# Performance work log

Measured on AMD Instinct MI355X. Metric: run time of the kernel, lower is better.

Reference implementation:

```python
import jax, jax.numpy as jnp
import numpy as np

N, H, S = 2048, 512, 256

def setup_inputs() -> dict:
    key = jax.random.key(0)
    k1, k2, k3 = jax.random.split(key, 3)
    hidden_states = jax.random.normal(k1, (N, H, S), dtype=jnp.float32)
    # xavier_uniform-ish scale for W and context vector
    limW = float(np.sqrt(6.0 / (H + H)))
    attention_weights = jax.random.uniform(k2, (H, H), dtype=jnp.float32, minval=-limW, maxval=limW)
    attention_bias = jnp.zeros((H, 1), dtype=jnp.float32)
    limc = float(np.sqrt(6.0 / (H + 1)))
    context_vector = jax.random.uniform(k3, (H, 1), dtype=jnp.float32, minval=-limc, maxval=limc)
    return {
        "hidden_states": hidden_states,
        "attention_weights": attention_weights,
        "attention_bias": attention_bias,
        "context_vector": context_vector,
    }

def reference(hidden_states, attention_weights, attention_bias, context_vector):
    # hidden_states: (N, H, S)
    hs_t = jnp.swapaxes(hidden_states, 1, 2)              # (N, S, H)
    score = jnp.tanh(hs_t @ attention_weights + attention_bias[:, 0])  # (N, S, H)
    alignment = (score @ context_vector)[..., 0]          # (N, S)
    attn = jax.nn.softmax(alignment, axis=1)              # (N, S)
    context = jnp.einsum('ns,nhs->nh', attn, hidden_states)  # (N, H)
    return context
```

## Files before the change

kernel.cpp:

```cpp
#include <hip/hip_runtime.h>
#include <hip/hip_bf16.h>
#include <stdint.h>
#include <stddef.h>

typedef __attribute__((ext_vector_type(8))) short short8;
typedef __attribute__((ext_vector_type(4))) float f32x4;

#define NB 2048
#define HD 512
#define SD 256

__device__ __forceinline__ short f2bf(float x) {
  __hip_bfloat16 h = __float2bfloat16(x);
  return *reinterpret_cast<short*>(&h);
}

__device__ __forceinline__ float fast_tanh(float x) {
  x = fminf(fmaxf(x, -15.f), 15.f);
  float e = __expf(2.f * x);
  return __fdividef(e - 1.f, e + 1.f);
}

__global__ __launch_bounds__(256) void wconv_kernel(const float* __restrict__ W,
                                                    short* __restrict__ Wtb) {
  __shared__ float tile[32][33];
  const int bx = blockIdx.x;
  const int tk0 = (bx & 15) * 32;
  const int tj0 = (bx >> 4) * 32;
  const int lx = threadIdx.x & 31;
  const int ly = threadIdx.x >> 5;
  for (int r = 0; r < 4; ++r) {
    int yy = ly + r * 8;
    tile[yy][lx] = W[(size_t)(tk0 + yy) * HD + tj0 + lx];
  }
  __syncthreads();
  const int kb = tk0 >> 5;
  for (int r = 0; r < 4; ++r) {
    int yy = ly + r * 8;
    Wtb[(size_t)kb * (HD * 32) + (size_t)(tj0 + yy) * 32 + lx] = f2bf(tile[lx][yy]);
  }
}

__global__ void __launch_bounds__(256, 2)
align_kernel(const float* __restrict__ hs, const short* __restrict__ Wtb,
             const float* __restrict__ bias, const float* __restrict__ ctx,
             float* __restrict__ align_out)
{
  __shared__ float abuf[64];

  const int tid = threadIdx.x;
  const int n = blockIdx.x >> 2;
  const int s0 = (blockIdx.x & 3) * 64;
  const int lane = tid & 63;
  const int wid = tid >> 6;
  const int l15 = lane & 15;
  const int lg = lane >> 4;
  const int jb = wid * 128;

  if (tid < 64) abuf[tid] = 0.f;
  __syncthreads();

  const float* hsA = hs + (size_t)n * (HD * SD) + s0 + l15 + (size_t)(lg * 8) * SD;
  const short* wbase = Wtb + (size_t)(jb + l15) * 32 + lg * 8;

  f32x4 acc[4][8];
  #pragma unroll
  for (int i = 0; i < 4; ++i)
    #pragma unroll
    for (int p = 0; p < 8; ++p)
      acc[i][p] = (f32x4){0.f, 0.f, 0.f, 0.f};

  for (int kt = 0; kt < 16; ++kt) {
    short8 wf[8];
    const short* wk = wbase + (size_t)kt * (HD * 32);
    #pragma unroll
    for (int p = 0; p < 8; ++p)
      wf[p] = *(const short8*)(wk + p * (16 * 32));

    short8 af[4];
    const float* ak = hsA + (size_t)(kt * 32) * SD;
    #pragma unroll
    for (int i = 0; i < 4; ++i) {
      float v[8];
      #pragma unroll
      for (int e = 0; e < 8; ++e)
        v[e] = ak[(size_t)e * SD + i * 16];
      short8 pk;
      #pragma unroll
      for (int e = 0; e < 8; ++e) pk[e] = f2bf(v[e]);
      af[i] = pk;
    }

    #pragma unroll
    for (int i = 0; i < 4; ++i)
      #pragma unroll
      for (int p = 0; p < 8; ++p)
        acc[i][p] = __builtin_amdgcn_mfma_f32_16x16x32_bf16(wf[p], af[i], acc[i][p], 0, 0, 0);
  }

  float part[4] = {0.f, 0.f, 0.f, 0.f};
  #pragma unroll
  for (int p = 0; p < 8; ++p) {
    const int j = jb + p * 16 + lg * 4;
    f32x4 bv = *(const f32x4*)(bias + j);
    f32x4 cv = *(const f32x4*)(ctx + j);
    #pragma unroll
    for (int i = 0; i < 4; ++i)
      #pragma unroll
      for (int r = 0; r < 4; ++r)
        part[i] += fast_tanh(acc[i][p][r] + bv[r]) * cv[r];
  }
  #pragma unroll
  for (int i = 0; i < 4; ++i) {
    part[i] += __shfl_xor(part[i], 16);
    part[i] += __shfl_xor(part[i], 32);
  }
  if (lg == 0) {
    #pragma unroll
    for (int i = 0; i < 4; ++i)
      atomicAdd(&abuf[i * 16 + l15], part[i]);
  }
  __syncthreads();
  if (tid < 64) align_out[(size_t)n * SD + s0 + tid] = abuf[tid];
}

__global__ __launch_bounds__(256) void ctx_kernel(const float* __restrict__ hs,
                                                  const float* __restrict__ align_in,
                                                  float* __restrict__ out)
{
  __shared__ __align__(16) float attn_s[256];
  __shared__ float red[8];
  const int n = blockIdx.x;
  const int t = threadIdx.x;
  const int lane = t & 63, wid = t >> 6;

  float a = align_in[(size_t)n * 256 + t];
  float m = a;
  #pragma unroll
  for (int off = 32; off; off >>= 1) m = fmaxf(m, __shfl_xor(m, off));
  if (lane == 0) red[wid] = m;
  __syncthreads();
  m = fmaxf(fmaxf(red[0], red[1]), fmaxf(red[2], red[3]));
  float e = __expf(a - m);
  float s = e;
  #pragma unroll
  for (int off = 32; off; off >>= 1) s += __shfl_xor(s, off);
  if (lane == 0) red[4 + wid] = s;
  __syncthreads();
  s = red[4] + red[5] + red[6] + red[7];
  attn_s[t] = e / s;
  __syncthreads();

  const int grp = t & 7;
  const int hrow = t >> 3;
  float av[32];
  #pragma unroll
  for (int u = 0; u < 8; ++u) {
    float4 v = *(const float4*)&attn_s[grp * 32 + u * 4];
    av[4*u+0] = v.x; av[4*u+1] = v.y; av[4*u+2] = v.z; av[4*u+3] = v.w;
  }
  const float* hb = hs + (size_t)n * (HD * SD) + grp * 32;
  for (int it = 0; it < 16; ++it) {
    const int h = it * 32 + hrow;
    const float4* p = (const float4*)(hb + (size_t)h * SD);
    float acc = 0.f;
    #pragma unroll
    for (int u = 0; u < 8; ++u) {
      float4 v = p[u];
      acc += av[4*u+0]*v.x + av[4*u+1]*v.y + av[4*u+2]*v.z + av[4*u+3]*v.w;
    }
    acc += __shfl_xor(acc, 1);
    acc += __shfl_xor(acc, 2);
    acc += __shfl_xor(acc, 4);
    if (grp == 0) out[(size_t)n * HD + h] = acc;
  }
}

extern "C" void kernel_launch(void* const* d_in, const int* in_sizes, int n_in,
                              void* d_out, int out_size, void* d_ws, size_t ws_size,
                              hipStream_t stream) {
  (void)in_sizes; (void)n_in; (void)out_size; (void)ws_size;
  const float* hs = (const float*)d_in[0];
  const float* W  = (const float*)d_in[1];
  const float* b  = (const float*)d_in[2];
  const float* c  = (const float*)d_in[3];
  float* out = (float*)d_out;

  float* align_ws = (float*)d_ws;
  short* Wtb = (short*)((char*)d_ws + (size_t)NB * SD * 4);

  wconv_kernel<<<256, 256, 0, stream>>>(W, Wtb);
  align_kernel<<<NB * 4, 256, 0, stream>>>(hs, Wtb, b, c, align_ws);
  ctx_kernel<<<NB, 256, 0, stream>>>(hs, align_ws, out);
}
```

Before: 846.8 us.

## Pre-transpose hidden states to bf16 (N,S,H) and double-buffer the align MFMA loop

Adds a tiled transpose kernel that converts hidden_states to a bf16 (N,S,H) workspace buffer. The alignment kernel can then load contiguous short8 fragments instead of doing strided scalar fp32 loads and per-element conversion. The MFMA k-loop is also double-buffered so the next tile's fragments load while the current tile computes. The cost is an extra full pass over the input (a 1 GB read plus a 0.5 GB write) and a large workspace requirement. When the workspace is too small, the code falls back to a chunked path or to the original kernel.

```diff
diff --git a/kernel.cpp b/kernel.cpp
--- a/kernel.cpp
+++ b/kernel.cpp
@@ -41,13 +41,142 @@
   }
 }
 
+__global__ __launch_bounds__(256) void tconv_kernel(const float* __restrict__ hs,
+                                                    short* __restrict__ hst,
+                                                    int nbase) {
+  __shared__ float tile[64][65];
+  const int bx = blockIdx.x;
+  const int nl = bx >> 5;
+  const int n = nbase + nl;
+  const int h0 = ((bx >> 2) & 7) * 64;
+  const int s0 = (bx & 3) * 64;
+  const int t = threadIdx.x;
+
+  const int lh = t >> 2;
+  const int lq = t & 3;
+  const float* src = hs + (size_t)n * (HD * SD) + (size_t)(h0 + lh) * SD + s0;
+  #pragma unroll
+  for (int r = 0; r < 4; ++r) {
+    const int q = lq + r * 4;
+    float4 v = *(const float4*)(src + q * 4);
+    tile[lh][q * 4 + 0] = v.x;
+    tile[lh][q * 4 + 1] = v.y;
+    tile[lh][q * 4 + 2] = v.z;
+    tile[lh][q * 4 + 3] = v.w;
+  }
+  __syncthreads();
+
+  const int ls = t >> 2;
+  const int lo = t & 3;
+  short* dst = hst + (size_t)nl * (SD * HD) + (size_t)(s0 + ls) * HD + h0;
+  #pragma unroll
+  for (int r = 0; r < 2; ++r) {
+    const int oct = lo + r * 4;
+    short8 pk;
+    #pragma unroll
+    for (int e = 0; e < 8; ++e)
+      pk[e] = f2bf(tile[oct * 8 + e][ls]);
+    *(short8*)(dst + oct * 8) = pk;
+  }
+}
+
 __global__ void __launch_bounds__(256, 2)
-align_kernel(const float* __restrict__ hs, const short* __restrict__ Wtb,
-             const float* __restrict__ bias, const float* __restrict__ ctx,
-             float* __restrict__ align_out)
+align_fast(const short* __restrict__ hst, const short* __restrict__ Wtb,
+           const float* __restrict__ bias, const float* __restrict__ ctx,
+           float* __restrict__ align_out, int nbase)
 {
   __shared__ float abuf[64];
 
+  const int tid = threadIdx.x;
+  const int nl = blockIdx.x >> 2;
+  const int n = nbase + nl;
+  const int s0 = (blockIdx.x & 3) * 64;
+  const int lane = tid & 63;
+  const int wid = tid >> 6;
+  const int l15 = lane & 15;
+  const int lg = lane >> 4;
+  const int jb = wid * 128;
+
+  if (tid < 64) abuf[tid] = 0.f;
+  __syncthreads();
+
+  const short* aBase = hst + (size_t)nl * (SD * HD) + (size_t)(s0 + l15) * HD + lg * 8;
+  const short* wBase = Wtb + (size_t)(jb + l15) * 32 + lg * 8;
+
+  f32x4 acc[4][8];
+  #pragma unroll
+  for (int i = 0; i < 4; ++i)
+    #pragma unroll
+    for (int p = 0; p < 8; ++p)
+      acc[i][p] = (f32x4){0.f, 0.f, 0.f, 0.f};
+
+  short8 afA[4], wfA[8], afB[4], wfB[8];
+  #pragma unroll
+  for (int i = 0; i < 4; ++i) afA[i] = *(const short8*)(aBase + i * 16 * HD);
+  #pragma unroll
+  for (int p = 0; p < 8; ++p) wfA[p] = *(const short8*)(wBase + p * (16 * 32));
+
+  for (int kt = 0; kt < 16; kt += 2) {
+    {
+      const short* ak = aBase + (kt + 1) * 32;
+      #pragma unroll
+      for (int i = 0; i < 4; ++i) afB[i] = *(const short8*)(ak + i * 16 * HD);
+      const short* wk = wBase + (size_t)(kt + 1) * (HD * 32);
+      #pragma unroll
+      for (int p = 0; p < 8; ++p) wfB[p] = *(const short8*)(wk + p * (16 * 32));
+    }
+    #pragma unroll
+    for (int i = 0; i < 4; ++i)
+      #pragma unroll
+      for (int p = 0; p < 8; ++p)
+        acc[i][p] = __builtin_amdgcn_mfma_f32_16x16x32_bf16(wfA[p], afA[i], acc[i][p], 0, 0, 0);
+    if (kt < 14) {
+      const short* ak = aBase + (kt + 2) * 32;
+      #pragma unroll
+      for (int i = 0; i < 4; ++i) afA[i] = *(const short8*)(ak + i * 16 * HD);
+      const short* wk = wBase + (size_t)(kt + 2) * (HD * 32);
+      #pragma unroll
+      for (int p = 0; p < 8; ++p) wfA[p] = *(const short8*)(wk + p * (16 * 32));
+    }
+    #pragma unroll
+    for (int i = 0; i < 4; ++i)
+      #pragma unroll
+      for (int p = 0; p < 8; ++p)
+        acc[i][p] = __builtin_amdgcn_mfma_f32_16x16x32_bf16(wfB[p], afB[i], acc[i][p], 0, 0, 0);
+  }
+
+  float part[4] = {0.f, 0.f, 0.f, 0.f};
+  #pragma unroll
+  for (int p = 0; p < 8; ++p) {
+    const int j = jb + p * 16 + lg * 4;
+    f32x4 bv = *(const f32x4*)(bias + j);
+    f32x4 cv = *(const f32x4*)(ctx + j);
+    #pragma unroll
+    for (int i = 0; i < 4; ++i)
+      #pragma unroll
+      for (int r = 0; r < 4; ++r)
+        part[i] += fast_tanh(acc[i][p][r] + bv[r]) * cv[r];
+  }
+  #pragma unroll
+  for (int i = 0; i < 4; ++i) {
+    part[i] += __shfl_xor(part[i], 16);
+    part[i] += __shfl_xor(part[i], 32);
+  }
+  if (lg == 0) {
+    #pragma unroll
+    for (int i = 0; i < 4; ++i)
+      atomicAdd(&abuf[i * 16 + l15], part[i]);
+  }
+  __syncthreads();
+  if (tid < 64) align_out[(size_t)n * SD + s0 + tid] = abuf[tid];
+}
+
+__global__ void __launch_bounds__(256, 2)
+align_fallback(const float* __restrict__ hs, const short* __restrict__ Wtb,
+               const float* __restrict__ bias, const float* __restrict__ ctx,
+               float* __restrict__ align_out)
+{
+  __shared__ float abuf[64];
   const int tid = threadIdx.x;
   const int n = blockIdx.x >> 2;
   const int s0 = (blockIdx.x & 3) * 64;
@@ -179,17 +308,37 @@
 extern "C" void kernel_launch(void* const* d_in, const int* in_sizes, int n_in,
                               void* d_out, int out_size, void* d_ws, size_t ws_size,
                               hipStream_t stream) {
-  (void)in_sizes; (void)n_in; (void)out_size; (void)ws_size;
+  (void)in_sizes; (void)n_in; (void)out_size;
   const float* hs = (const float*)d_in[0];
   const float* W  = (const float*)d_in[1];
   const float* b  = (const float*)d_in[2];
   const float* c  = (const float*)d_in[3];
   float* out = (float*)d_out;
 
-  float* align_ws = (float*)d_ws;
-  short* Wtb = (short*)((char*)d_ws + (size_t)NB * SD * 4);
+  const size_t OFF_ALIGN = 0;
+  const size_t OFF_WTB   = (size_t)NB * SD * 4;
+  const size_t OFF_HST   = OFF_WTB + (size_t)16 * HD * 32 * 2;
+  const size_t HST_FULL  = (size_t)NB * SD * HD * 2;
+  const size_t HST_CHUNK = HST_FULL / 8;
+
+  float* align_ws = (float*)((char*)d_ws + OFF_ALIGN);
+  short* Wtb = (short*)((char*)d_ws + OFF_WTB);
+  short* hst = (short*)((char*)d_ws + OFF_HST);
 
   wconv_kernel<<<256, 256, 0, stream>>>(W, Wtb);
-  align_kernel<<<NB * 4, 256, 0, stream>>>(hs, Wtb, b, c, align_ws);
+
+  if (ws_size >= OFF_HST + HST_FULL) {
+    tconv_kernel<<<NB * 32, 256, 0, stream>>>(hs, hst, 0);
+    align_fast<<<NB * 4, 256, 0, stream>>>(hst, Wtb, b, c, align_ws, 0);
+  } else if (ws_size >= OFF_HST + HST_CHUNK) {
+    for (int chunk = 0; chunk < 8; ++chunk) {
+      const int nbase = chunk * (NB / 8);
+      tconv_kernel<<<(NB / 8) * 32, 256, 0, stream>>>(hs, hst, nbase);
+      align_fast<<<(NB / 8) * 4, 256, 0, stream>>>(hst, Wtb, b, c, align_ws, nbase);
+    }
+  } else {
+    align_fallback<<<NB * 4, 256, 0, stream>>>(hs, Wtb, b, c, align_ws);
+  }
+
   ctx_kernel<<<NB, 256, 0, stream>>>(hs, align_ws, out);
 }
```

Result: slower. 1.265 ms (+49.4%).

## Stage hidden-state and weight tiles in LDS with double buffering in align kernel

Applied to the files above, without the earlier changes.

The align kernel now uses 1024-thread blocks covering 128 sequence positions and all 512 output columns. Each k-step's bf16 activation tile and weight tile are loaded cooperatively into double-buffered shared memory, so every global element is fetched once per block instead of once per wave. The next tile's global loads are issued before the current tile's MFMAs. This cuts redundant global traffic for W and gives coalesced staging of hs, at the cost of a block-wide barrier every k-step and about 80KB of LDS per block, which may limit occupancy.

```diff
diff --git a/kernel.cpp b/kernel.cpp
--- a/kernel.cpp
+++ b/kernel.cpp
@@ -4,6 +4,7 @@
 #include <stddef.h>
 
 typedef __attribute__((ext_vector_type(8))) short short8;
+typedef __attribute__((ext_vector_type(4))) short short4v;
 typedef __attribute__((ext_vector_type(4))) float f32x4;
 
 #define NB 2048
@@ -41,69 +42,104 @@
   }
 }
 
-__global__ void __launch_bounds__(256, 2)
+__global__ void __launch_bounds__(1024, 4)
 align_kernel(const float* __restrict__ hs, const short* __restrict__ Wtb,
-             const float* __restrict__ bias, const float* __restrict__ ctx,
+             const float* __restrict__ bias, const float* __restrict__ ctxv,
              float* __restrict__ align_out)
 {
-  __shared__ float abuf[64];
+  __shared__ short As[2][128 * 32];
+  __shared__ short Ws[2][512 * 32];
+  __shared__ float abuf[128];
 
   const int tid = threadIdx.x;
-  const int n = blockIdx.x >> 2;
-  const int s0 = (blockIdx.x & 3) * 64;
+  const int n = blockIdx.x >> 1;
+  const int s0 = (blockIdx.x & 1) * 128;
+  const float* hsn = hs + (size_t)n * (HD * SD) + s0;
+
+  if (tid < 128) abuf[tid] = 0.f;
+
+  const int a_s = tid >> 3;
+  const int a_o = (tid >> 1) & 3;
+  const int a_h = tid & 1;
+  const int a_k = a_o * 8 + a_h * 4;
+  const int w_j = tid >> 1;
+  const int w_o = (tid & 1) * 2;
+
+  {
+    const float* src = hsn + (size_t)a_k * SD + a_s;
+    short4v pk;
+    #pragma unroll
+    for (int e = 0; e < 4; ++e) pk[e] = f2bf(src[(size_t)e * SD]);
+    *(short4v*)&As[0][a_s * 32 + a_k] = pk;
+
+    const short* wsrc = Wtb + (size_t)w_j * 32 + w_o * 8;
+    *(short8*)&Ws[0][w_j * 32 + w_o * 8] = *(const short8*)(wsrc);
+    *(short8*)&Ws[0][w_j * 32 + w_o * 8 + 8] = *(const short8*)(wsrc + 8);
+  }
+  __syncthreads();
+
   const int lane = tid & 63;
   const int wid = tid >> 6;
+  const int wm = wid >> 3;
+  const int wj = wid & 7;
   const int l15 = lane & 15;
   const int lg = lane >> 4;
-  const int jb = wid * 128;
-
-  if (tid < 64) abuf[tid] = 0.f;
-  __syncthreads();
-
-  const float* hsA = hs + (size_t)n * (HD * SD) + s0 + l15 + (size_t)(lg * 8) * SD;
-  const short* wbase = Wtb + (size_t)(jb + l15) * 32 + lg * 8;
-
-  f32x4 acc[4][8];
+
+  f32x4 acc[4][4];
   #pragma unroll
   for (int i = 0; i < 4; ++i)
     #pragma unroll
-    for (int p = 0; p < 8; ++p)
+    for (int p = 0; p < 4; ++p)
       acc[i][p] = (f32x4){0.f, 0.f, 0.f, 0.f};
 
+  const int aoff = (wm * 64 + l15) * 32 + lg * 8;
+  const int woff = (wj * 64 + l15) * 32 + lg * 8;
+
   for (int kt = 0; kt < 16; ++kt) {
-    short8 wf[8];
-    const short* wk = wbase + (size_t)kt * (HD * 32);
-    #pragma unroll
-    for (int p = 0; p < 8; ++p)
-      wf[p] = *(const short8*)(wk + p * (16 * 32));
-
-    short8 af[4];
-    const float* ak = hsA + (size_t)(kt * 32) * SD;
+    const int cur = kt & 1;
+
+    float av[4];
+    short8 wv0, wv1;
+    if (kt < 15) {
+      const float* src = hsn + (size_t)((kt + 1) * 32 + a_k) * SD + a_s;
+      #pragma unroll
+      for (int e = 0; e < 4; ++e) av[e] = src[(size_t)e * SD];
+      const short* wsrc = Wtb + (size_t)(kt + 1) * (HD * 32) + w_j * 32 + w_o * 8;
+      wv0 = *(const short8*)(wsrc);
+      wv1 = *(const short8*)(wsrc + 8);
+    }
+
+    short8 wf[4];
+    #pragma unroll
+    for (int p = 0; p < 4; ++p)
+      wf[p] = *(const short8*)&Ws[cur][woff + p * (16 * 32)];
+
     #pragma unroll
     for (int i = 0; i < 4; ++i) {
-      float v[8];
-      #pragma unroll
-      for (int e = 0; e < 8; ++e)
-        v[e] = ak[(size_t)e * SD + i * 16];
-      short8 pk;
-      #pragma unroll
-      for (int e = 0; e < 8; ++e) pk[e] = f2bf(v[e]);
-      af[i] = pk;
-    }
-
-    #pragma unroll
-    for (int i = 0; i < 4; ++i)
-      #pragma unroll
-      for (int p = 0; p < 8; ++p)
-        acc[i][p] = __builtin_amdgcn_mfma_f32_16x16x32_bf16(wf[p], af[i], acc[i][p], 0, 0, 0);
+      short8 af = *(const short8*)&As[cur][aoff + i * (16 * 32)];
+      #pragma unroll
+      for (int p = 0; p < 4; ++p)
+        acc[i][p] = __builtin_amdgcn_mfma_f32_16x16x32_bf16(wf[p], af, acc[i][p], 0, 0, 0);
+    }
+
+    if (kt < 15) {
+      const int nxt = cur ^ 1;
+      short4v pk;
+      #pragma unroll
+      for (int e = 0; e < 4; ++e) pk[e] = f2bf(av[e]);
+      *(short4v*)&As[nxt][a_s * 32 + a_k] = pk;
+      *(short8*)&Ws[nxt][w_j * 32 + w_o * 8] = wv0;
+      *(short8*)&Ws[nxt][w_j * 32 + w_o * 8 + 8] = wv1;
+    }
+    __syncthreads();
   }
 
   float part[4] = {0.f, 0.f, 0.f, 0.f};
   #pragma unroll
-  for (int p = 0; p < 8; ++p) {
-    const int j = jb + p * 16 + lg * 4;
+  for (int p = 0; p < 4; ++p) {
+    const int j = wj * 64 + p * 16 + lg * 4;
     f32x4 bv = *(const f32x4*)(bias + j);
-    f32x4 cv = *(const f32x4*)(ctx + j);
+    f32x4 cv = *(const f32x4*)(ctxv + j);
     #pragma unroll
     for (int i = 0; i < 4; ++i)
       #pragma unroll
@@ -118,10 +154,10 @@
   if (lg == 0) {
     #pragma unroll
     for (int i = 0; i < 4; ++i)
-      atomicAdd(&abuf[i * 16 + l15], part[i]);
-  }
-  __syncthreads();
-  if (tid < 64) align_out[(size_t)n * SD + s0 + tid] = abuf[tid];
+      atomicAdd(&abuf[wm * 64 + i * 16 + l15], part[i]);
+  }
+  __syncthreads();
+  if (tid < 128) align_out[(size_t)n * SD + s0 + tid] = abuf[tid];
 }
 
 __global__ __launch_bounds__(256) void ctx_kernel(const float* __restrict__ hs,
@@ -190,6 +226,6 @@
   short* Wtb = (short*)((char*)d_ws + (size_t)NB * SD * 4);
 
   wconv_kernel<<<256, 256, 0, stream>>>(W, Wtb);
-  align_kernel<<<NB * 4, 256, 0, stream>>>(hs, Wtb, b, c, align_ws);
+  align_kernel<<<NB * 2, 1024, 0, stream>>>(hs, Wtb, b, c, align_ws);
   ctx_kernel<<<NB, 256, 0, stream>>>(hs, align_ws, out);
 }
```

Result: slower. 944.7 us (median of 2 runs) (+11.6%).

## Stage A and W tiles in double-buffered LDS and use 32x32x16 MFMA

Applied to the files above, without the earlier changes.

The align kernel now runs 512 threads per block and stages bf16-converted hidden-state and weight K-slices in double-buffered shared memory. The next slice is prefetched into registers while the current one feeds 32x32x16 MFMAs, and the weight layout is re-blocked into K groups of 16. This replaces per-wave direct global loads, with their redundant W fetches and strided hs reads, by cooperative loads and LDS reuse. In exchange it adds a barrier every K step, doubles the K iterations, and uses more LDS, which may limit occupancy.

```diff
diff --git a/kernel.cpp b/kernel.cpp
--- a/kernel.cpp
+++ b/kernel.cpp
@@ -4,11 +4,16 @@
 #include <stddef.h>
 
 typedef __attribute__((ext_vector_type(8))) short short8;
+typedef __attribute__((ext_vector_type(4))) short short4v;
 typedef __attribute__((ext_vector_type(4))) float f32x4;
+typedef __attribute__((ext_vector_type(16))) float f32x16;
 
 #define NB 2048
 #define HD 512
 #define SD 256
+
+#define AS_STR 24
+#define WS_STR 24
 
 __device__ __forceinline__ short f2bf(float x) {
   __hip_bfloat16 h = __float2bfloat16(x);
@@ -22,7 +27,7 @@
 }
 
 __global__ __launch_bounds__(256) void wconv_kernel(const float* __restrict__ W,
-                                                    short* __restrict__ Wtb) {
+                                                    short* __restrict__ Wtb16) {
   __shared__ float tile[32][33];
   const int bx = blockIdx.x;
   const int tk0 = (bx & 15) * 32;
@@ -34,91 +39,129 @@
     tile[yy][lx] = W[(size_t)(tk0 + yy) * HD + tj0 + lx];
   }
   __syncthreads();
-  const int kb = tk0 >> 5;
   for (int r = 0; r < 4; ++r) {
     int yy = ly + r * 8;
-    Wtb[(size_t)kb * (HD * 32) + (size_t)(tj0 + yy) * 32 + lx] = f2bf(tile[lx][yy]);
-  }
-}
-
-__global__ void __launch_bounds__(256, 2)
-align_kernel(const float* __restrict__ hs, const short* __restrict__ Wtb,
-             const float* __restrict__ bias, const float* __restrict__ ctx,
+    const int k = tk0 + lx;
+    Wtb16[(size_t)(k >> 4) * (HD * 16) + (size_t)(tj0 + yy) * 16 + (k & 15)] =
+        f2bf(tile[lx][yy]);
+  }
+}
+
+__global__ void __launch_bounds__(512, 4)
+align_kernel(const float* __restrict__ hs, const short* __restrict__ Wtb16,
+             const float* __restrict__ bias, const float* __restrict__ ctxv,
              float* __restrict__ align_out)
 {
+  __shared__ short As[2][64 * AS_STR];
+  __shared__ short Ws[2][512 * WS_STR];
   __shared__ float abuf[64];
 
   const int tid = threadIdx.x;
   const int n = blockIdx.x >> 2;
   const int s0 = (blockIdx.x & 3) * 64;
+  const float* hsn = hs + (size_t)n * (HD * SD) + s0;
+
+  if (tid < 64) abuf[tid] = 0.f;
+
+  const int a_s = tid & 63;
+  const int a_kq = (tid >> 6) & 3;
+  const int w_j = tid;
+
+  if (tid < 256) {
+    const float* src = hsn + (size_t)(a_kq * 4) * SD + a_s;
+    short4v pk;
+    pk[0] = f2bf(src[0]); pk[1] = f2bf(src[SD]);
+    pk[2] = f2bf(src[2 * SD]); pk[3] = f2bf(src[3 * SD]);
+    *(short4v*)&As[0][a_s * AS_STR + a_kq * 4] = pk;
+  }
+  {
+    const short* wsrc = Wtb16 + (size_t)w_j * 16;
+    *(short8*)&Ws[0][w_j * WS_STR] = *(const short8*)wsrc;
+    *(short8*)&Ws[0][w_j * WS_STR + 8] = *(const short8*)(wsrc + 8);
+  }
+  __syncthreads();
+
   const int lane = tid & 63;
   const int wid = tid >> 6;
-  const int l15 = lane & 15;
-  const int lg = lane >> 4;
-  const int jb = wid * 128;
-
-  if (tid < 64) abuf[tid] = 0.f;
-  __syncthreads();
-
-  const float* hsA = hs + (size_t)n * (HD * SD) + s0 + l15 + (size_t)(lg * 8) * SD;
-  const short* wbase = Wtb + (size_t)(jb + l15) * 32 + lg * 8;
-
-  f32x4 acc[4][8];
-  #pragma unroll
-  for (int i = 0; i < 4; ++i)
+  const int jb = wid * 64;
+  const int l31 = lane & 31;
+  const int hg = lane >> 5;
+
+  f32x16 acc[2][2];
+  #pragma unroll
+  for (int i = 0; i < 2; ++i)
     #pragma unroll
-    for (int p = 0; p < 8; ++p)
-      acc[i][p] = (f32x4){0.f, 0.f, 0.f, 0.f};
-
-  for (int kt = 0; kt < 16; ++kt) {
-    short8 wf[8];
-    const short* wk = wbase + (size_t)kt * (HD * 32);
+    for (int p = 0; p < 2; ++p)
+      #pragma unroll
+      for (int q = 0; q < 16; ++q) acc[i][p][q] = 0.f;
+
+  const int afo = l31 * AS_STR + hg * 8;
+  const int wfo = (jb + l31) * WS_STR + hg * 8;
+
+  for (int kt = 0; kt < 32; ++kt) {
+    const int cur = kt & 1;
+
+    float av[4];
+    short8 wv0, wv1;
+    if (kt < 31) {
+      if (tid < 256) {
+        const float* src = hsn + (size_t)((kt + 1) * 16 + a_kq * 4) * SD + a_s;
+        #pragma unroll
+        for (int e = 0; e < 4; ++e) av[e] = src[(size_t)e * SD];
+      }
+      const short* wsrc = Wtb16 + (size_t)(kt + 1) * (HD * 16) + (size_t)w_j * 16;
+      wv0 = *(const short8*)wsrc;
+      wv1 = *(const short8*)(wsrc + 8);
+    }
+
+    short8 wf0 = *(const short8*)&Ws[cur][wfo];
+    short8 wf1 = *(const short8*)&Ws[cur][wfo + 32 * WS_STR];
+    short8 af0 = *(const short8*)&As[cur][afo];
+    short8 af1 = *(const short8*)&As[cur][afo + 32 * AS_STR];
+
+    __builtin_amdgcn_s_setprio(1);
+    acc[0][0] = __builtin_amdgcn_mfma_f32_32x32x16_bf16(wf0, af0, acc[0][0], 0, 0, 0);
+    acc[0][1] = __builtin_amdgcn_mfma_f32_32x32x16_bf16(wf1, af0, acc[0][1], 0, 0, 0);
+    acc[1][0] = __builtin_amdgcn_mfma_f32_32x32x16_bf16(wf0, af1, acc[1][0], 0, 0, 0);
+    acc[1][1] = __builtin_amdgcn_mfma_f32_32x32x16_bf16(wf1, af1, acc[1][1], 0, 0, 0);
+    __builtin_amdgcn_s_setprio(0);
+
+    if (kt < 31) {
+      const int nxt = cur ^ 1;
+      if (tid < 256) {
+        short4v pk;
+        #pragma unroll
+        for (int e = 0; e < 4; ++e) pk[e] = f2bf(av[e]);
+        *(short4v*)&As[nxt][a_s * AS_STR + a_kq * 4] = pk;
+      }
+      *(short8*)&Ws[nxt][w_j * WS_STR] = wv0;
+      *(short8*)&Ws[nxt][w_j * WS_STR + 8] = wv1;
+    }
+    __syncthreads();
+  }
+
+  float part0 = 0.f, part1 = 0.f;
+  #pragma unroll
+  for (int p = 0; p < 2; ++p) {
+    const int jfr = jb + p * 32 + hg * 4;
     #pragma unroll
-    for (int p = 0; p < 8; ++p)
-      wf[p] = *(const short8*)(wk + p * (16 * 32));
-
-    short8 af[4];
-    const float* ak = hsA + (size_t)(kt * 32) * SD;
-    #pragma unroll
-    for (int i = 0; i < 4; ++i) {
-      float v[8];
+    for (int g = 0; g < 4; ++g) {
+      const int j4 = jfr + g * 8;
+      f32x4 bv = *(const f32x4*)(bias + j4);
+      f32x4 cv = *(const f32x4*)(ctxv + j4);
       #pragma unroll
-      for (int e = 0; e < 8; ++e)
-        v[e] = ak[(size_t)e * SD + i * 16];
-      short8 pk;
-      #pragma unroll
-      for (int e = 0; e < 8; ++e) pk[e] = f2bf(v[e]);
-      af[i] = pk;
-    }
-
-    #pragma unroll
-    for (int i = 0; i < 4; ++i)
-      #pragma unroll
-      for (int p = 0; p < 8; ++p)
-        acc[i][p] = __builtin_amdgcn_mfma_f32_16x16x32_bf16(wf[p], af[i], acc[i][p], 0, 0, 0);
-  }
-
-  float part[4] = {0.f, 0.f, 0.f, 0.f};
-  #pragma unroll
-  for (int p = 0; p < 8; ++p) {
-    const int j = jb + p * 16 + lg * 4;
-    f32x4 bv = *(const f32x4*)(bias + j);
-    f32x4 cv = *(const f32x4*)(ctx + j);
-    #pragma unroll
-    for (int i = 0; i < 4; ++i)
-      #pragma unroll
-      for (int r = 0; r < 4; ++r)
-        part[i] += fast_tanh(acc[i][p][r] + bv[r]) * cv[r];
-  }
-  #pragma unroll
-  for (int i = 0; i < 4; ++i) {
-    part[i] += __shfl_xor(part[i], 16);
-    part[i] += __shfl_xor(part[i], 32);
-  }
-  if (lg == 0) {
-    #pragma unroll
-    for (int i = 0; i < 4; ++i)
-      atomicAdd(&abuf[i * 16 + l15], part[i]);
+      for (int r = 0; r < 4; ++r) {
+        const int q = g * 4 + r;
+        part0 += fast_tanh(acc[0][p][q] + bv[r]) * cv[r];
+        part1 += fast_tanh(acc[1][p][q] + bv[r]) * cv[r];
+      }
+    }
+  }
+  part0 += __shfl_xor(part0, 32);
+  part1 += __shfl_xor(part1, 32);
+  if (lane < 32) {
+    atomicAdd(&abuf[l31], part0);
+    atomicAdd(&abuf[32 + l31], part1);
   }
   __syncthreads();
   if (tid < 64) align_out[(size_t)n * SD + s0 + tid] = abuf[tid];
@@ -187,9 +230,9 @@
   float* out = (float*)d_out;
 
   float* align_ws = (float*)d_ws;
-  short* Wtb = (short*)((char*)d_ws + (size_t)NB * SD * 4);
-
-  wconv_kernel<<<256, 256, 0, stream>>>(W, Wtb);
-  align_kernel<<<NB * 4, 256, 0, stream>>>(hs, Wtb, b, c, align_ws);
+  short* Wtb16 = (short*)((char*)d_ws + (size_t)NB * SD * 4);
+
+  wconv_kernel<<<256, 256, 0, stream>>>(W, Wtb16);
+  align_kernel<<<NB * 4, 512, 0, stream>>>(hs, Wtb16, b, c, align_ws);
   ctx_kernel<<<NB, 256, 0, stream>>>(hs, align_ws, out);
 }
```

New measurement: 806.3 us. 4.8% less time.
